# Optimization experiments

Measured on AMD Instinct MI355X. Metric: run time of the kernel, lower is better.

The kernel has to match this reference:

```python
import jax, jax.numpy as jnp
import numpy as np
import math

N, C, T, V = 8, 256, 128, 25
H, HC = 8, 32            # num_heads, head_channels
W, DIL = 3, 1            # window, dilation
O = 256                  # out_channels
PAD = (W + (W - 1) * (DIL - 1) - 1) // 2
B, L = N * T, W * V


def _ln(x, g, b):
    m = jnp.mean(x, -1, keepdims=True)
    v = jnp.var(x, -1, keepdims=True)
    return (x - m) * jax.lax.rsqrt(v + 1e-5) * g + b


def setup_inputs() -> dict:
    key = jax.random.key(0)
    ks = iter(jax.random.split(key, 40))
    def w(shape):
        return jax.random.normal(next(ks), shape, jnp.float32) * 0.02
    d = {"x": jax.random.normal(next(ks), (N, C, T, V), jnp.float32)}
    d.update(
        ln1_g=jnp.ones((C,)), ln1_b=jnp.zeros((C,)),
        Wq=w((C, C)), bq=jnp.zeros((C,)), Wqa=w((C, H)), bqa=jnp.zeros((H,)),
        Wk=w((C, C)), bk=jnp.zeros((C,)), Wka=w((C, H)), bka=jnp.zeros((H,)),
        Wv=w((C, C)), bv=jnp.zeros((C,)), Wt=w((C, C)), bt=jnp.zeros((C,)),
        Wp=w((C, C)), bp=jnp.zeros((C,)),
        ffn_g=jnp.ones((C,)), ffn_b=jnp.zeros((C,)),
        W1=w((C, C)), b1=jnp.zeros((C,)), W2=w((C, C)), b2=jnp.zeros((C,)),
        tn_g=jnp.ones((C,)), tn_b=jnp.zeros((C,)),
        c1_w=w((C, O)), c1_b=jnp.zeros((O,)),
        c2_w=w((W, O, O)), c2_b=jnp.zeros((O,)),
    )
    return d


def reference(x, ln1_g, ln1_b, Wq, bq, Wqa, bqa, Wk, bk, Wka, bka, Wv, bv,
              Wt, bt, Wp, bp, ffn_g, ffn_b, W1, b1, W2, b2, tn_g, tn_b,
              c1_w, c1_b, c2_w, c2_b):
    scale = 1.0 / math.sqrt(HC)
    # ---- Unfold over time: build window of frames around each t (nn.Unfold) ----
    xp = jnp.pad(x, ((0, 0), (0, 0), (PAD, PAD), (0, 0)))
    win = jnp.stack([jax.lax.dynamic_slice_in_dim(xp, k * DIL, T, 2) for k in range(W)], 2)  # (N,C,W,T,V)
    seq = win.transpose(0, 3, 2, 4, 1).reshape(B, L, C)  # (N*T, W*V, C)

    sep = lambda z: z.reshape(B, L, H, HC).transpose(0, 2, 1, 3)  # (B,H,L,HC)
    grp = lambda z: z.transpose(0, 2, 1, 3).reshape(B, -1, C)

    # ---- SpatioTemporalAttention (eval: dropouts off) ----
    nx = _ln(seq, ln1_g, ln1_b)
    q = nx @ Wq + bq                                            # (B,L,C)
    qw = jax.nn.softmax((q @ Wqa + bqa).transpose(0, 2, 1) * scale, axis=-1)  # (B,H,L)
    pq = jnp.einsum('bhl,bhlc->bhc', qw, sep(q)).reshape(B, 1, C)             # pooled query
    keys = nx @ Wk + bk
    kw = jax.nn.softmax(((keys * pq) @ Wka + bka).transpose(0, 2, 1) * scale, axis=-1)
    pk = jnp.einsum('bhl,bhlc->bhc', kw, sep(keys))             # pooled key (B,H,HC)
    vals = sep(nx @ Wv + bv)
    kv = grp(vals * pk[:, :, None, :]) @ Wt + bt                # (B,L,C)
    attn = (kv + q) @ Wp + bp                                   # residual-in-heads == plain add

    # ---- AttentionBranch residual + FFN ----
    att = attn + seq
    f = _ln(att, ffn_g, ffn_b)
    y = jax.nn.gelu(f @ W1 + b1, approximate=False) @ W2 + b2 + att  # (B,L,C)

    # ---- temporal branch: LN -> regroup frames -> 1x1 conv -> GELU -> (W,1) conv stride W ----
    t5 = _ln(y, tn_g, tn_b).reshape(N, T, W, V, C)
    h = jax.nn.gelu(t5 @ c1_w + c1_b, approximate=False)        # (N,T,W,V,O)
    out = jnp.einsum('ntwvi,wio->ntvo', h, c2_w) + c2_b         # stride==kernel conv == window contraction
    return out.transpose(0, 3, 1, 2)                            # (N,O,T,V)
```

## Files before the change

kernel.cpp:

```cpp
#include <hip/hip_runtime.h>


#define DI __device__ __forceinline__

constexpr int CC   = 256;
constexpr int CL   = 75;
constexpr int CV   = 25;
constexpr int CT   = 128;
constexpr int TP   = 130;
constexpr int MPAD = 8 * TP * CV;
constexpr int MBL  = 1024 * CL;
constexpr int MOUT = 8 * CT * CV;
constexpr float SM_SCALE = 0.17677669529663687f;

typedef __bf16 bf16x8 __attribute__((ext_vector_type(8)));
typedef float f32x4 __attribute__((ext_vector_type(4)));

DI float bf2f(unsigned short u) { return __uint_as_float(((unsigned)u) << 16); }
DI float bf2f_lo(unsigned u) { return __uint_as_float(u << 16); }
DI float bf2f_hi(unsigned u) { return __uint_as_float(u & 0xffff0000u); }
DI unsigned short f2bf(float f) {
  unsigned u = __float_as_uint(f);
  u += 0x7fffu + ((u >> 16) & 1u);
  return (unsigned short)(u >> 16);
}
DI unsigned packbf(float a, float b) {
  return (unsigned)f2bf(a) | ((unsigned)f2bf(b) << 16);
}
DI float geluf(float x) { return 0.5f * x * (1.f + erff(x * 0.70710678118654752440f)); }

DI void gll16(const unsigned short* g, unsigned short* l) {
  __builtin_amdgcn_global_load_lds(
      (const __attribute__((address_space(1))) unsigned int*)g,
      (__attribute__((address_space(3))) unsigned int*)l, 16, 0, 0);
}

DI int arow(int r) {
  int b = r / CL;
  int l = r - b * CL;
  int w = l / CV;
  int v = l - w * CV;
  int t = b & (CT - 1);
  int n = b >> 7;
  return (n * TP + t + w) * CV + v;
}

__global__ __launch_bounds__(256) void k_transpose(const float* __restrict__ x,
                                                   unsigned short* __restrict__ xtp) {
  __shared__ float tile[32][33];
  const int n = blockIdx.z;
  const int c0 = blockIdx.x * 32;
  const int tv0 = blockIdx.y * 32;
  const int tx = threadIdx.x & 31, ty = threadIdx.x >> 5;
#pragma unroll
  for (int j = 0; j < 32; j += 8) {
    tile[ty + j][tx] = x[((size_t)(n * CC + c0 + ty + j)) * 3200 + tv0 + tx];
  }
  __syncthreads();
#pragma unroll
  for (int j = 0; j < 32; j += 8) {
    int tv = tv0 + ty + j;
    int st = tv / CV, v = tv - st * CV;
    size_t row = ((size_t)n * TP + st + 1) * CV + v;
    xtp[row * CC + c0 + tx] = f2bf(tile[tx][ty + j]);
  }
}

__global__ __launch_bounds__(256) void k_zero_pad(unsigned short* __restrict__ xtp) {
  int i = blockIdx.x * 256 + threadIdx.x;
  int c = i & 255;
  int rid = i >> 8;
  int n = rid / 50;
  int rem = rid - n * 50;
  int side = rem / 25;
  int v = rem - side * 25;
  size_t row = ((size_t)n * TP + side * (TP - 1)) * CV + v;
  xtp[row * CC + c] = 0;
}

struct TJobs {
  const float* src[10];
  unsigned short* dst[10];
  int stride[10];
  int off[10];
};
__global__ __launch_bounds__(256) void k_wtrans(TJobs J) {
  __shared__ float tile[32][33];
  const int j = blockIdx.z;
  const float* src = J.src[j];
  unsigned short* dst = J.dst[j];
  const int stride = J.stride[j], off = J.off[j];
  const int k0 = blockIdx.x * 32, n0 = blockIdx.y * 32;
  const int tx = threadIdx.x & 31, ty = threadIdx.x >> 5;
#pragma unroll
  for (int jj = 0; jj < 32; jj += 8)
    tile[ty + jj][tx] = src[(size_t)(k0 + ty + jj) * 256 + n0 + tx];
  __syncthreads();
#pragma unroll
  for (int jj = 0; jj < 32; jj += 8)
    dst[(size_t)(n0 + ty + jj) * stride + off + k0 + tx] = f2bf(tile[tx][ty + jj]);
}

__global__ __launch_bounds__(256) void k_wtwp(const float* __restrict__ Wt,
                                              const float* __restrict__ Wp,
                                              unsigned short* __restrict__ fused) {
  __shared__ float wrow[256];
  const int k = blockIdx.x, n = threadIdx.x;
  wrow[n] = Wt[(size_t)k * 256 + n];
  __syncthreads();
  float acc = 0.f;
  for (int j = 0; j < 256; ++j) acc = fmaf(wrow[j], Wp[(size_t)j * 256 + n], acc);
  fused[(size_t)n * 512 + k] = f2bf(acc);
}

__global__ __launch_bounds__(256) void k_bias2(const float* __restrict__ bt,
                                               const float* __restrict__ Wp,
                                               const float* __restrict__ bp,
                                               const float* __restrict__ bq,
                                               const float* __restrict__ bk,
                                               const float* __restrict__ bv,
                                               float* __restrict__ bias2,
                                               float* __restrict__ bias3) {
  const int n = threadIdx.x;
  float acc = bp[n];
  for (int j = 0; j < 256; ++j) acc = fmaf(bt[j], Wp[(size_t)j * 256 + n], acc);
  bias2[n] = acc;
  bias3[n] = bq[n];
  bias3[256 + n] = bk[n];
  bias3[512 + n] = bv[n];
}

__global__ __launch_bounds__(256) void k_ln4(const unsigned short* __restrict__ X,
                                             const float* __restrict__ g,
                                             const float* __restrict__ b,
                                             unsigned short* __restrict__ Y) {
  const int row = blockIdx.x * 4 + (threadIdx.x >> 6);
  const int lane = threadIdx.x & 63;
  const uint2 u = *(const uint2*)(X + (size_t)row * CC + lane * 4);
  const float x0 = bf2f_lo(u.x), x1 = bf2f_hi(u.x), x2 = bf2f_lo(u.y), x3 = bf2f_hi(u.y);
  float s = x0 + x1 + x2 + x3;
  float q = x0 * x0 + x1 * x1 + x2 * x2 + x3 * x3;
#pragma unroll
  for (int o = 32; o; o >>= 1) { s += __shfl_xor(s, o); q += __shfl_xor(q, o); }
  const float mean = s * (1.f / CC);
  const float var = q * (1.f / CC) - mean * mean;
  const float rs = rsqrtf(var + 1e-5f);
  const float4 g4 = *(const float4*)(g + lane * 4);
  const float4 b4 = *(const float4*)(b + lane * 4);
  uint2 o2;
  o2.x = packbf((x0 - mean) * rs * g4.x + b4.x, (x1 - mean) * rs * g4.y + b4.y);
  o2.y = packbf((x2 - mean) * rs * g4.z + b4.z, (x3 - mean) * rs * g4.w + b4.w);
  *(uint2*)(Y + (size_t)row * CC + lane * 4) = o2;
}

template <int AMODE, int EPI, int KD, bool MULTI>
__global__ __launch_bounds__(512) void k_mgemm(const unsigned short* __restrict__ A,
                                               const unsigned short* __restrict__ BwT,
                                               const float* __restrict__ bias,
                                               unsigned short* __restrict__ Cout,
                                               float* __restrict__ FOut,
                                               int M) {
  if constexpr (MULTI) {
    const int z = blockIdx.y;
    BwT += (size_t)z * (256 * 256);
    bias += z * 256;
    Cout += (size_t)z * MPAD * CC;
  }
  __shared__ unsigned short SH[20480];
  const int tid = threadIdx.x;
  const int lane = tid & 63;
  const int wid = tid >> 6;
  const int wm = wid >> 2, wn = wid & 3;
  const int r0 = blockIdx.x * 64;
  f32x4 acc[2][4] = {};

  const bool sa = tid < 256;
  const int rA = r0 + (tid >> 2);
  const int rAc = (rA < M) ? rA : (M - 1);
  const int segs = ((tid & 3) ^ ((tid >> 3) & 3)) * 8;
  int hrb = 0;
  if (sa && AMODE == 4 && rA < M) {
    const int nb = rA / 3200, rr = rA - nb * 3200;
    const int tq = rr / 25, vq = rr - tq * 25;
    hrb = (nb * CT + tq) * CL + vq;
  }

  auto loadA4 = [&](int k0) -> uint4 {
    uint4 u = make_uint4(0, 0, 0, 0);
    if (!(sa && rA < M)) return u;
    const int w = k0 >> 8;
    u = *(const uint4*)(A + (size_t)(hrb + w * CV) * CC + (k0 & 255) + segs);
    return u;
  };
  auto stageB = [&](int buf, int k0) {
    unsigned short* bs = SH + 4096 + buf * 8192;
#pragma unroll
    for (int pp = 0; pp < 2; ++pp) {
      const int s = tid + pp * 512;
      const int cs = ((s & 3) ^ ((s >> 3) & 3)) * 8;
      gll16(BwT + (size_t)(s >> 2) * KD + k0 + cs, bs + s * 8);
    }
  };
  auto stageAg = [&](int buf, int k0) {
    if (sa) gll16(A + (size_t)rAc * CC + k0 + segs, SH + buf * 2048 + tid * 8);
  };
  const int swl = ((lane & 15) >> 1) & 3;
  auto mfmaStep = [&](int cur) {
    const unsigned short* as = SH + cur * 2048;
    const unsigned short* bs = SH + 4096 + cur * 8192;
    bf16x8 af[2], bfr[4];
#pragma unroll
    for (int mi = 0; mi < 2; ++mi)
      af[mi] = *(const bf16x8*)(as + (wm * 32 + mi * 16 + (lane & 15)) * 32 +
                                (((lane >> 4) ^ swl) * 8));
#pragma unroll
    for (int ni = 0; ni < 4; ++ni)
      bfr[ni] = *(const bf16x8*)(bs + (wn * 64 + ni * 16 + (lane & 15)) * 32 +
                                 (((lane >> 4) ^ swl) * 8));
#pragma unroll
    for (int mi = 0; mi < 2; ++mi)
#pragma unroll
      for (int ni = 0; ni < 4; ++ni)
        acc[mi][ni] = __builtin_amdgcn_mfma_f32_16x16x32_bf16(af[mi], bfr[ni], acc[mi][ni], 0, 0, 0);
  };

  constexpr int NT = KD / 32;
  if constexpr (AMODE == 0) {
    asm volatile("s_waitcnt vmcnt(0)" ::: "memory");
    stageB(0, 0);
    stageAg(0, 0);
    for (int t = 0; t < NT; ++t) {
      const int cur = t & 1;
      const bool more = (t + 1 < NT);
      if (more) { stageB(cur ^ 1, (t + 1) * 32); stageAg(cur ^ 1, (t + 1) * 32); }
      if (wid < 4) {
        if (more) asm volatile("s_waitcnt vmcnt(3)" ::: "memory");
        else      asm volatile("s_waitcnt vmcnt(0)" ::: "memory");
      } else {
        if (more) asm volatile("s_waitcnt vmcnt(2)" ::: "memory");
        else      asm volatile("s_waitcnt vmcnt(0)" ::: "memory");
      }
      __builtin_amdgcn_s_barrier();
      asm volatile("" ::: "memory");
      mfmaStep(cur);
      asm volatile("s_waitcnt lgkmcnt(0)" ::: "memory");
      __builtin_amdgcn_s_barrier();
      asm volatile("" ::: "memory");
    }
    __syncthreads();
  } else {
    {
      const uint4 a0 = loadA4(0);
      stageB(0, 0);
      if (sa) *(uint4*)(SH + tid * 8) = a0;
    }
    for (int t = 0; t < NT; ++t) {
      const int cur = t & 1;
      const bool more = (t + 1 < NT);
      if (more) {
        const uint4 an = loadA4((t + 1) * 32);
        stageB(cur ^ 1, (t + 1) * 32);
        if (sa) *(uint4*)(SH + (cur ^ 1) * 2048 + tid * 8) = an;
      }
      asm volatile("s_waitcnt lgkmcnt(0)" ::: "memory");
      if (more) asm volatile("s_waitcnt vmcnt(2)" ::: "memory");
      else      asm volatile("s_waitcnt vmcnt(0)" ::: "memory");
      __builtin_amdgcn_s_barrier();
      asm volatile("" ::: "memory");
      mfmaStep(cur);
      asm volatile("s_waitcnt lgkmcnt(0)" ::: "memory");
      __builtin_amdgcn_s_barrier();
      asm volatile("" ::: "memory");
    }
    if constexpr (EPI == 0) __syncthreads();
  }

  const int ln15 = lane & 15, lq = lane >> 4;
  if constexpr (EPI == 4) {
#pragma unroll
    for (int mi = 0; mi < 2; ++mi) {
#pragma unroll
      for (int ni = 0; ni < 4; ++ni) {
        const int col = wn * 64 + ni * 16 + ln15;
        const float bcol = bias[col];
        const int rbase = r0 + wm * 32 + mi * 16 + lq * 4;
        const int nb = rbase / 3200, rr = rbase - nb * 3200;
        float4 v;
        v.x = acc[mi][ni][0] + bcol;
        v.y = acc[mi][ni][1] + bcol;
        v.z = acc[mi][ni][2] + bcol;
        v.w = acc[mi][ni][3] + bcol;
        *(float4*)(FOut + (size_t)nb * 819200 + (size_t)col * 3200 + rr) = v;
      }
    }
  } else {
    constexpr int LDC = 260;
#pragma unroll
    for (int mi = 0; mi < 2; ++mi) {
#pragma unroll
      for (int ni = 0; ni < 4; ++ni) {
        const int col = wn * 64 + ni * 16 + ln15;
        const float bcol = bias[col];
#pragma unroll
        for (int rg = 0; rg < 4; ++rg) {
          const int lrow = wm * 32 + mi * 16 + lq * 4 + rg;
          SH[lrow * LDC + col] = f2bf(acc[mi][ni][rg] + bcol);
        }
      }
    }
    __syncthreads();
#pragma unroll
    for (int i = 0; i < 4; ++i) {
      const int idx = tid + i * 512;
      const int row = idx >> 5, ch = idx & 31;
      const int gr = r0 + row;
      if (gr < M)
        *(uint4*)(Cout + (size_t)gr * CC + ch * 8) = *(const uint4*)&SH[row * LDC + ch * 8];
    }
  }
}

__global__ __launch_bounds__(512, 4) void k_chain(
    const unsigned short* __restrict__ VP, const unsigned short* __restrict__ QP,
    const float* __restrict__ PK, const unsigned short* __restrict__ XTP,
    const unsigned short* __restrict__ fusedB, const float* __restrict__ bias2,
    const unsigned short* __restrict__ W1T, const float* __restrict__ b1,
    const unsigned short* __restrict__ W2T, const float* __restrict__ b2,
    const float* __restrict__ ffn_g, const float* __restrict__ ffn_b,
    const unsigned short* __restrict__ c1wT, const float* __restrict__ c1b,
    const float* __restrict__ tn_g, const float* __restrict__ tn_b,
    unsigned short* __restrict__ Hout) {
  constexpr int LDC = 264;
  __shared__ unsigned short SH[16896 + 4096 + 16384];
  unsigned short* ACT = SH;
  unsigned short* AS = SH + 16896;
  unsigned short* BS = SH + 16896 + 4096;
  const int tid = threadIdx.x;
  const int lane = tid & 63, wid = tid >> 6;
  const int wm = wid >> 2, wn = wid & 3;
  const int ln15 = lane & 15, lq = lane >> 4;
  const int swl = (ln15 >> 1) & 3;
  const int r0 = blockIdx.x * 64;

  const bool sa = tid < 256;
  const int rA = r0 + (tid >> 2);
  const int segs = ((tid & 3) ^ ((tid >> 3) & 3)) * 8;
  int ar = 0, bb = 0;
  if (sa) { ar = arow(rA); bb = rA / CL; }
  int xrow[8];
#pragma unroll
  for (int i = 0; i < 8; ++i)
    xrow[i] = arow(r0 + wm * 32 + (i >> 2) * 16 + lq * 4 + (i & 3));

  auto stageB = [&](const unsigned short* BwT, int KD, int buf, int k0) {
    unsigned short* bs = BS + buf * 8192;
#pragma unroll
    for (int pp = 0; pp < 2; ++pp) {
      const int s = tid + pp * 512;
      const int cs = ((s & 3) ^ ((s >> 3) & 3)) * 8;
      gll16(BwT + (size_t)(s >> 2) * KD + k0 + cs, bs + s * 8);
    }
  };
  auto loadA5 = [&](int k0) -> uint4 {
    uint4 u = make_uint4(0, 0, 0, 0);
    if (!sa) return u;
    if (k0 < 256) {
      const int kg = k0 + segs;
      const uint4 t4 = *(const uint4*)(VP + (size_t)ar * CC + kg);
      const float* sv = PK + bb * CC + kg;
      const float4 s0 = *(const float4*)sv;
      const float4 s1 = *(const float4*)(sv + 4);
      u.x = packbf(bf2f_lo(t4.x) * s0.x, bf2f_hi(t4.x) * s0.y);
      u.y = packbf(bf2f_lo(t4.y) * s0.z, bf2f_hi(t4.y) * s0.w);
      u.z = packbf(bf2f_lo(t4.z) * s1.x, bf2f_hi(t4.z) * s1.y);
      u.w = packbf(bf2f_lo(t4.w) * s1.z, bf2f_hi(t4.w) * s1.w);
    } else {
      u = *(const uint4*)(QP + (size_t)ar * CC + (k0 - 256) + segs);
    }
    return u;
  };
  auto ln_inplace = [&](const float* g, const float* b) {
    const float4 g4 = *(const float4*)(g + lane * 4);
    const float4 b4 = *(const float4*)(b + lane * 4);
#pragma unroll
    for (int rr = 0; rr < 8; ++rr) {
      const int row = wid * 8 + rr;
      const uint2 u = *(const uint2*)(ACT + row * LDC + lane * 4);
      const float x0 = bf2f_lo(u.x), x1 = bf2f_hi(u.x);
      const float x2 = bf2f_lo(u.y), x3 = bf2f_hi(u.y);
      float s = x0 + x1 + x2 + x3;
      float q = x0 * x0 + x1 * x1 + x2 * x2 + x3 * x3;
#pragma unroll
      for (int o = 32; o; o >>= 1) { s += __shfl_xor(s, o); q += __shfl_xor(q, o); }
      const float mean = s * (1.f / CC);
      const float var = q * (1.f / CC) - mean * mean;
      const float rs = rsqrtf(var + 1e-5f);
      uint2 o2;
      o2.x = packbf((x0 - mean) * rs * g4.x + b4.x, (x1 - mean) * rs * g4.y + b4.y);
      o2.y = packbf((x2 - mean) * rs * g4.z + b4.z, (x3 - mean) * rs * g4.w + b4.w);
      *(uint2*)(ACT + row * LDC + lane * 4) = o2;
    }
  };
  auto gemmACT = [&](const unsigned short* BwT, f32x4 (&a)[2][4], bool prestaged) {
    if (!prestaged) {
      asm volatile("s_waitcnt vmcnt(0)" ::: "memory");
      stageB(BwT, 256, 0, 0);
    }
    for (int t = 0; t < 8; ++t) {
      const int cur = t & 1;
      const bool more = (t + 1 < 8);
      if (more) stageB(BwT, 256, cur ^ 1, (t + 1) * 32);
      bf16x8 af[2];
#pragma unroll
      for (int mi = 0; mi < 2; ++mi)
        af[mi] = *(const bf16x8*)(ACT + (wm * 32 + mi * 16 + ln15) * LDC + t * 32 + lq * 8);
      if (more) asm volatile("s_waitcnt vmcnt(2)" ::: "memory");
      else      asm volatile("s_waitcnt vmcnt(0)" ::: "memory");
      __builtin_amdgcn_s_barrier();
      asm volatile("" ::: "memory");
      bf16x8 bfr[4];
#pragma unroll
      for (int ni = 0; ni < 4; ++ni)
        bfr[ni] = *(const bf16x8*)(BS + cur * 8192 + (wn * 64 + ni * 16 + ln15) * 32 +
                                   ((lq ^ swl) * 8));
#pragma unroll
      for (int mi = 0; mi < 2; ++mi)
#pragma unroll
        for (int ni = 0; ni < 4; ++ni)
          a[mi][ni] = __builtin_amdgcn_mfma_f32_16x16x32_bf16(af[mi], bfr[ni], a[mi][ni], 0, 0, 0);
      asm volatile("s_waitcnt lgkmcnt(0)" ::: "memory");
      __builtin_amdgcn_s_barrier();
      asm volatile("" ::: "memory");
    }
  };

  f32x4 acc[2][4] = {};
  {
    const uint4 a0 = loadA5(0);
    stageB(fusedB, 512, 0, 0);
    if (sa) *(uint4*)(AS + tid * 8) = a0;
  }
  for (int t = 0; t < 16; ++t) {
    const int cur = t & 1;
    const bool more = (t + 1 < 16);
    if (more) {
      const uint4 an = loadA5((t + 1) * 32);
      stageB(fusedB, 512, cur ^ 1, (t + 1) * 32);
      if (sa) *(uint4*)(AS + (cur ^ 1) * 2048 + tid * 8) = an;
    }
    asm volatile("s_waitcnt lgkmcnt(0)" ::: "memory");
    if (more) asm volatile("s_waitcnt vmcnt(2)" ::: "memory");
    else      asm volatile("s_waitcnt vmcnt(0)" ::: "memory");
    __builtin_amdgcn_s_barrier();
    asm volatile("" ::: "memory");
    {
      bf16x8 af[2], bfr[4];
#pragma unroll
      for (int mi = 0; mi < 2; ++mi)
        af[mi] = *(const bf16x8*)(AS + cur * 2048 + (wm * 32 + mi * 16 + ln15) * 32 +
                                  ((lq ^ swl) * 8));
#pragma unroll
      for (int ni = 0; ni < 4; ++ni)
        bfr[ni] = *(const bf16x8*)(BS + cur * 8192 + (wn * 64 + ni * 16 + ln15) * 32 +
                                   ((lq ^ swl) * 8));
#pragma unroll
      for (int mi = 0; mi < 2; ++mi)
#pragma unroll
        for (int ni = 0; ni < 4; ++ni)
          acc[mi][ni] = __builtin_amdgcn_mfma_f32_16x16x32_bf16(af[mi], bfr[ni], acc[mi][ni], 0, 0, 0);
    }
    asm volatile("s_waitcnt lgkmcnt(0)" ::: "memory");
    __builtin_amdgcn_s_barrier();
    asm volatile("" ::: "memory");
  }
  stageB(W1T, 256, 0, 0);
  f32x4 attres[2][4];
#pragma unroll
  for (int mi = 0; mi < 2; ++mi) {
#pragma unroll
    for (int ni = 0; ni < 4; ++ni) {
      const int col = wn * 64 + ni * 16 + ln15;
      const float bcol = bias2[col];
#pragma unroll
      for (int rg = 0; rg < 4; ++rg) {
        attres[mi][ni][rg] =
            acc[mi][ni][rg] + bcol + bf2f(XTP[(size_t)xrow[mi * 4 + rg] * CC + col]);
        ACT[(wm * 32 + mi * 16 + lq * 4 + rg) * LDC + col] = f2bf(attres[mi][ni][rg]);
      }
    }
  }
  __syncthreads();
  ln_inplace(ffn_g, ffn_b);
  __syncthreads();

  f32x4 acc2[2][4] = {};
  gemmACT(W1T, acc2, true);
  stageB(W2T, 256, 0, 0);
  __syncthreads();
#pragma unroll
  for (int mi = 0; mi < 2; ++mi)
#pragma unroll
    for (int ni = 0; ni < 4; ++ni) {
      const int col = wn * 64 + ni * 16 + ln15;
      const float bcol = b1[col];
#pragma unroll
      for (int rg = 0; rg < 4; ++rg)
        ACT[(wm * 32 + mi * 16 + lq * 4 + rg) * LDC + col] = f2bf(geluf(acc2[mi][ni][rg] + bcol));
    }
  __syncthreads();

  f32x4 acc3[2][4] = {};
  gemmACT(W2T, acc3, true);
  stageB(c1wT, 256, 0, 0);
  __syncthreads();
#pragma unroll
  for (int mi = 0; mi < 2; ++mi)
#pragma unroll
    for (int ni = 0; ni < 4; ++ni) {
      const int col = wn * 64 + ni * 16 + ln15;
      const float bcol = b2[col];
#pragma unroll
      for (int rg = 0; rg < 4; ++rg)
        ACT[(wm * 32 + mi * 16 + lq * 4 + rg) * LDC + col] =
            f2bf(acc3[mi][ni][rg] + bcol + attres[mi][ni][rg]);
    }
  __syncthreads();
  ln_inplace(tn_g, tn_b);
  __syncthreads();

  f32x4 acc4[2][4] = {};
  gemmACT(c1wT, acc4, true);
  __syncthreads();
#pragma unroll
  for (int mi = 0; mi < 2; ++mi)
#pragma unroll
    for (int ni = 0; ni < 4; ++ni) {
      const int col = wn * 64 + ni * 16 + ln15;
      const float bcol = c1b[col];
#pragma unroll
      for (int rg = 0; rg < 4; ++rg)
        ACT[(wm * 32 + mi * 16 + lq * 4 + rg) * LDC + col] = f2bf(geluf(acc4[mi][ni][rg] + bcol));
    }
  __syncthreads();
#pragma unroll
  for (int i = 0; i < 4; ++i) {
    const int idx = tid + i * 512;
    const int row = idx >> 5, ch = idx & 31;
    *(uint4*)(Hout + (size_t)(r0 + row) * CC + ch * 8) = *(const uint4*)&ACT[row * LDC + ch * 8];
  }
}

__global__ __launch_bounds__(256) void k_attpool2(
    const unsigned short* __restrict__ QPr, const unsigned short* __restrict__ KPr,
    const float* __restrict__ Wqa, const float* __restrict__ bqa,
    const float* __restrict__ Wka, const float* __restrict__ bka,
    float* __restrict__ PK) {
  __shared__ unsigned short rows[CL * CC];
  __shared__ float uu[8 * 258];
  __shared__ float lg[8 * 76];
  __shared__ float inv8[8];
  __shared__ float pq[256];
  __shared__ int arl[CL];
  const int b = blockIdx.x;
  const int t = threadIdx.x;

  if (t < CL) arl[t] = arow(b * CL + t);
  __syncthreads();

  auto dot_phase = [&](const float* b8) {
    const int c0 = (t & 63) * 4;
    for (int i = t; i < CL * 8; i += 256) {
      const int h = i / CL, l = i - h * CL;
      float acc = b8[h];
#pragma unroll 4
      for (int jj = 0; jj < CC; jj += 4) {
        const int c = (c0 + jj) & 255;
        const uint2 pr = *(const uint2*)&rows[l * CC + c];
        acc = fmaf(bf2f_lo(pr.x), uu[h * 258 + c], acc);
        acc = fmaf(bf2f_hi(pr.x), uu[h * 258 + c + 1], acc);
        acc = fmaf(bf2f_lo(pr.y), uu[h * 258 + c + 2], acc);
        acc = fmaf(bf2f_hi(pr.y), uu[h * 258 + c + 3], acc);
      }
      lg[h * 76 + l] = acc * SM_SCALE;
    }
  };
  auto softmax8 = [&]() {
    if (t < 8) {
      float m = -1e30f;
      for (int l = 0; l < CL; ++l) m = fmaxf(m, lg[t * 76 + l]);
      float s = 0.f;
      for (int l = 0; l < CL; ++l) {
        const float e = __expf(lg[t * 76 + l] - m);
        lg[t * 76 + l] = e;
        s += e;
      }
      inv8[t] = 1.f / s;
    }
  };

  for (int i = t; i < CL * 32; i += 256) {
    const int r = i >> 5, seg = i & 31;
    gll16(QPr + (size_t)arl[r] * CC + seg * 8, &rows[i * 8]);
  }
  for (int i = t; i < CC * 8; i += 256) {
    const int c = i >> 3, h = i & 7;
    uu[h * 258 + c] = Wqa[c * 8 + h];
  }
  __syncthreads();
  dot_phase(bqa);
  __syncthreads();
  softmax8();
  __syncthreads();
  {
    const int h = t >> 5;
    float acc = 0.f;
    for (int l = 0; l < CL; ++l) acc = fmaf(lg[h * 76 + l], bf2f(rows[l * CC + t]), acc);
    pq[t] = acc * inv8[h];
  }
  __syncthreads();

  for (int i = t; i < CL * 32; i += 256) {
    const int r = i >> 5, seg = i & 31;
    gll16(KPr + (size_t)arl[r] * CC + seg * 8, &rows[i * 8]);
  }
  for (int i = t; i < CC * 8; i += 256) {
    const int c = i >> 3, h = i & 7;
    uu[h * 258 + c] = pq[c] * Wka[c * 8 + h];
  }
  __syncthreads();
  dot_phase(bka);
  __syncthreads();
  softmax8();
  __syncthreads();
  {
    const int h = t >> 5;
    float acc = 0.f;
    for (int l = 0; l < CL; ++l) acc = fmaf(lg[h * 76 + l], bf2f(rows[l * CC + t]), acc);
    PK[(size_t)b * CC + t] = acc * inv8[h];
  }
}

extern "C" void kernel_launch(void* const* d_in, const int* in_sizes, int n_in,
                              void* d_out, int out_size, void* d_ws, size_t ws_size,
                              hipStream_t stream) {
  const float* x = (const float*)d_in[0];
  const float* ln1_g = (const float*)d_in[1];
  const float* ln1_b = (const float*)d_in[2];
  const float* Wq = (const float*)d_in[3];
  const float* bq = (const float*)d_in[4];
  const float* Wqa = (const float*)d_in[5];
  const float* bqa = (const float*)d_in[6];
  const float* Wk = (const float*)d_in[7];
  const float* bk = (const float*)d_in[8];
  const float* Wka = (const float*)d_in[9];
  const float* bka = (const float*)d_in[10];
  const float* Wv = (const float*)d_in[11];
  const float* bv = (const float*)d_in[12];
  const float* Wt = (const float*)d_in[13];
  const float* bt = (const float*)d_in[14];
  const float* Wp = (const float*)d_in[15];
  const float* bp = (const float*)d_in[16];
  const float* ffn_g = (const float*)d_in[17];
  const float* ffn_b = (const float*)d_in[18];
  const float* W1 = (const float*)d_in[19];
  const float* b1 = (const float*)d_in[20];
  const float* W2 = (const float*)d_in[21];
  const float* b2 = (const float*)d_in[22];
  const float* tn_g = (const float*)d_in[23];
  const float* tn_b = (const float*)d_in[24];
  const float* c1w = (const float*)d_in[25];
  const float* c1b = (const float*)d_in[26];
  const float* c2w = (const float*)d_in[27];
  const float* c2b = (const float*)d_in[28];
  float* out = (float*)d_out;

  char* wp = (char*)d_ws;
  auto alloc = [&](size_t bytes) -> char* {
    char* p = wp;
    wp += (bytes + 255) & ~(size_t)255;
    return p;
  };
  unsigned short* XTP = (unsigned short*)alloc((size_t)MPAD * CC * 2);
  unsigned short* LNXP = (unsigned short*)alloc((size_t)MPAD * CC * 2);
  unsigned short* QKVP = (unsigned short*)alloc((size_t)3 * MPAD * CC * 2);
  unsigned short* QP = QKVP;
  unsigned short* KP = QKVP + (size_t)MPAD * CC;
  unsigned short* VP = QKVP + (size_t)2 * MPAD * CC;
  unsigned short* Hb = (unsigned short*)alloc((size_t)MBL * CC * 2);
  float* PK = (float*)alloc((size_t)1024 * CC * 4);
  unsigned short* WqkvT = (unsigned short*)alloc((size_t)3 * 256 * 256 * 2);
  unsigned short* W1T = (unsigned short*)alloc(256 * 256 * 2);
  unsigned short* W2T = (unsigned short*)alloc(256 * 256 * 2);
  unsigned short* c1wT = (unsigned short*)alloc(256 * 256 * 2);
  unsigned short* c2wT = (unsigned short*)alloc(256 * 768 * 2);
  unsigned short* fusedB = (unsigned short*)alloc(256 * 512 * 2);
  float* bias2 = (float*)alloc(256 * 4);
  float* bias3 = (float*)alloc(768 * 4);

  TJobs J;
  const float* srcs[10] = {Wq, Wk, Wv, W1, W2, c1w, c2w, c2w + 65536, c2w + 131072, Wp};
  unsigned short* dsts[10] = {WqkvT, WqkvT + 65536, WqkvT + 131072, W1T, W2T, c1wT,
                              c2wT, c2wT, c2wT, fusedB};
  const int strides[10] = {256, 256, 256, 256, 256, 256, 768, 768, 768, 512};
  const int offs[10] = {0, 0, 0, 0, 0, 0, 0, 256, 512, 256};
  for (int i = 0; i < 10; ++i) {
    J.src[i] = srcs[i]; J.dst[i] = dsts[i]; J.stride[i] = strides[i]; J.off[i] = offs[i];
  }
  k_wtrans<<<dim3(8, 8, 10), 256, 0, stream>>>(J);
  k_wtwp<<<256, 256, 0, stream>>>(Wt, Wp, fusedB);
  k_bias2<<<1, 256, 0, stream>>>(bt, Wp, bp, bq, bk, bv, bias2, bias3);

  k_transpose<<<dim3(8, 100, 8), 256, 0, stream>>>(x, XTP);
  k_zero_pad<<<400, 256, 0, stream>>>(XTP);
  k_ln4<<<MPAD / 4, 256, 0, stream>>>(XTP, ln1_g, ln1_b, LNXP);

  const int gP = (MPAD + 63) / 64;
  const int gO = MOUT / 64;
  k_mgemm<0, 0, 256, true><<<dim3(gP, 3), 512, 0, stream>>>(
      LNXP, WqkvT, bias3, QKVP, nullptr, MPAD);

  k_attpool2<<<1024, 256, 0, stream>>>(QP, KP, Wqa, bqa, Wka, bka, PK);

  k_chain<<<MBL / 64, 512, 0, stream>>>(VP, QP, PK, XTP, fusedB, bias2,
                                        W1T, b1, W2T, b2, ffn_g, ffn_b,
                                        c1wT, c1b, tn_g, tn_b, Hb);

  k_mgemm<4, 4, 768, false><<<gO, 512, 0, stream>>>(Hb, c2wT, c2b, nullptr, out, MOUT);
}
```

Before: 265.7 us.

## Precompute q·Wp in the deduplicated QKV GEMM to halve the chain GEMM K

Folds Wq·Wp into a fourth output slice of the padded-frame QKV projection, with bias bq·Wp, so the q@Wp contribution is computed once per padded frame row rather than per windowed row. The attention chain GEMM's K dimension drops from 512 to 256, and the precomputed term is added from memory in the residual epilogue. This adds a larger QKV GEMM grid, an extra bf16 intermediate buffer and read, and a slight change in rounding.

```diff
diff --git a/kernel.cpp b/kernel.cpp
--- a/kernel.cpp
+++ b/kernel.cpp
@@ -79,10 +79,10 @@
 }
 
 struct TJobs {
-  const float* src[10];
-  unsigned short* dst[10];
-  int stride[10];
-  int off[10];
+  const float* src[9];
+  unsigned short* dst[9];
+  int stride[9];
+  int off[9];
 };
 __global__ __launch_bounds__(256) void k_wtrans(TJobs J) {
   __shared__ float tile[32][33];
@@ -102,15 +102,19 @@
 }
 
 __global__ __launch_bounds__(256) void k_wtwp(const float* __restrict__ Wt,
+                                              const float* __restrict__ Wq,
                                               const float* __restrict__ Wp,
-                                              unsigned short* __restrict__ fused) {
+                                              unsigned short* __restrict__ fusedB,
+                                              unsigned short* __restrict__ WqWpT) {
   __shared__ float wrow[256];
   const int k = blockIdx.x, n = threadIdx.x;
-  wrow[n] = Wt[(size_t)k * 256 + n];
+  const float* src = blockIdx.y ? Wq : Wt;
+  unsigned short* dst = blockIdx.y ? WqWpT : fusedB;
+  wrow[n] = src[(size_t)k * 256 + n];
   __syncthreads();
   float acc = 0.f;
   for (int j = 0; j < 256; ++j) acc = fmaf(wrow[j], Wp[(size_t)j * 256 + n], acc);
-  fused[(size_t)n * 512 + k] = f2bf(acc);
+  dst[(size_t)n * 256 + k] = f2bf(acc);
 }
 
 __global__ __launch_bounds__(256) void k_bias2(const float* __restrict__ bt,
@@ -123,11 +127,17 @@
                                                float* __restrict__ bias3) {
   const int n = threadIdx.x;
   float acc = bp[n];
-  for (int j = 0; j < 256; ++j) acc = fmaf(bt[j], Wp[(size_t)j * 256 + n], acc);
+  float accq = 0.f;
+  for (int j = 0; j < 256; ++j) {
+    const float w = Wp[(size_t)j * 256 + n];
+    acc = fmaf(bt[j], w, acc);
+    accq = fmaf(bq[j], w, accq);
+  }
   bias2[n] = acc;
   bias3[n] = bq[n];
   bias3[256 + n] = bk[n];
   bias3[512 + n] = bv[n];
+  bias3[768 + n] = accq;
 }
 
 __global__ __launch_bounds__(256) void k_ln4(const unsigned short* __restrict__ X,
@@ -321,8 +331,8 @@
 }
 
 __global__ __launch_bounds__(512, 4) void k_chain(
-    const unsigned short* __restrict__ VP, const unsigned short* __restrict__ QP,
-    const float* __restrict__ PK, const unsigned short* __restrict__ XTP,
+    const unsigned short* __restrict__ VP, const float* __restrict__ PK,
+    const unsigned short* __restrict__ XTP, const unsigned short* __restrict__ QWPP,
     const unsigned short* __restrict__ fusedB, const float* __restrict__ bias2,
     const unsigned short* __restrict__ W1T, const float* __restrict__ b1,
     const unsigned short* __restrict__ W2T, const float* __restrict__ b2,
@@ -364,19 +374,15 @@
   auto loadA5 = [&](int k0) -> uint4 {
     uint4 u = make_uint4(0, 0, 0, 0);
     if (!sa) return u;
-    if (k0 < 256) {
-      const int kg = k0 + segs;
-      const uint4 t4 = *(const uint4*)(VP + (size_t)ar * CC + kg);
-      const float* sv = PK + bb * CC + kg;
-      const float4 s0 = *(const float4*)sv;
-      const float4 s1 = *(const float4*)(sv + 4);
-      u.x = packbf(bf2f_lo(t4.x) * s0.x, bf2f_hi(t4.x) * s0.y);
-      u.y = packbf(bf2f_lo(t4.y) * s0.z, bf2f_hi(t4.y) * s0.w);
-      u.z = packbf(bf2f_lo(t4.z) * s1.x, bf2f_hi(t4.z) * s1.y);
-      u.w = packbf(bf2f_lo(t4.w) * s1.z, bf2f_hi(t4.w) * s1.w);
-    } else {
-      u = *(const uint4*)(QP + (size_t)ar * CC + (k0 - 256) + segs);
-    }
+    const int kg = k0 + segs;
+    const uint4 t4 = *(const uint4*)(VP + (size_t)ar * CC + kg);
+    const float* sv = PK + bb * CC + kg;
+    const float4 s0 = *(const float4*)sv;
+    const float4 s1 = *(const float4*)(sv + 4);
+    u.x = packbf(bf2f_lo(t4.x) * s0.x, bf2f_hi(t4.x) * s0.y);
+    u.y = packbf(bf2f_lo(t4.y) * s0.z, bf2f_hi(t4.y) * s0.w);
+    u.z = packbf(bf2f_lo(t4.z) * s1.x, bf2f_hi(t4.z) * s1.y);
+    u.w = packbf(bf2f_lo(t4.w) * s1.z, bf2f_hi(t4.w) * s1.w);
     return u;
   };
   auto ln_inplace = [&](const float* g, const float* b) {
@@ -437,15 +443,15 @@
   f32x4 acc[2][4] = {};
   {
     const uint4 a0 = loadA5(0);
-    stageB(fusedB, 512, 0, 0);
+    stageB(fusedB, 256, 0, 0);
     if (sa) *(uint4*)(AS + tid * 8) = a0;
   }
-  for (int t = 0; t < 16; ++t) {
+  for (int t = 0; t < 8; ++t) {
     const int cur = t & 1;
-    const bool more = (t + 1 < 16);
+    const bool more = (t + 1 < 8);
     if (more) {
       const uint4 an = loadA5((t + 1) * 32);
-      stageB(fusedB, 512, cur ^ 1, (t + 1) * 32);
+      stageB(fusedB, 256, cur ^ 1, (t + 1) * 32);
       if (sa) *(uint4*)(AS + (cur ^ 1) * 2048 + tid * 8) = an;
     }
     asm volatile("s_waitcnt lgkmcnt(0)" ::: "memory");
@@ -483,8 +489,8 @@
       const float bcol = bias2[col];
 #pragma unroll
       for (int rg = 0; rg < 4; ++rg) {
-        attres[mi][ni][rg] =
-            acc[mi][ni][rg] + bcol + bf2f(XTP[(size_t)xrow[mi * 4 + rg] * CC + col]);
+        const size_t ro = (size_t)xrow[mi * 4 + rg] * CC + col;
+        attres[mi][ni][rg] = acc[mi][ni][rg] + bcol + bf2f(QWPP[ro]) + bf2f(XTP[ro]);
         ACT[(wm * 32 + mi * 16 + lq * 4 + rg) * LDC + col] = f2bf(attres[mi][ni][rg]);
       }
     }
@@ -682,32 +688,33 @@
   };
   unsigned short* XTP = (unsigned short*)alloc((size_t)MPAD * CC * 2);
   unsigned short* LNXP = (unsigned short*)alloc((size_t)MPAD * CC * 2);
-  unsigned short* QKVP = (unsigned short*)alloc((size_t)3 * MPAD * CC * 2);
+  unsigned short* QKVP = (unsigned short*)alloc((size_t)4 * MPAD * CC * 2);
   unsigned short* QP = QKVP;
   unsigned short* KP = QKVP + (size_t)MPAD * CC;
   unsigned short* VP = QKVP + (size_t)2 * MPAD * CC;
+  unsigned short* QWPP = QKVP + (size_t)3 * MPAD * CC;
   unsigned short* Hb = (unsigned short*)alloc((size_t)MBL * CC * 2);
   float* PK = (float*)alloc((size_t)1024 * CC * 4);
-  unsigned short* WqkvT = (unsigned short*)alloc((size_t)3 * 256 * 256 * 2);
+  unsigned short* WqkvT = (unsigned short*)alloc((size_t)4 * 256 * 256 * 2);
   unsigned short* W1T = (unsigned short*)alloc(256 * 256 * 2);
   unsigned short* W2T = (unsigned short*)alloc(256 * 256 * 2);
   unsigned short* c1wT = (unsigned short*)alloc(256 * 256 * 2);
   unsigned short* c2wT = (unsigned short*)alloc(256 * 768 * 2);
-  unsigned short* fusedB = (unsigned short*)alloc(256 * 512 * 2);
+  unsigned short* fusedB = (unsigned short*)alloc(256 * 256 * 2);
   float* bias2 = (float*)alloc(256 * 4);
-  float* bias3 = (float*)alloc(768 * 4);
+  float* bias3 = (float*)alloc(1024 * 4);
 
   TJobs J;
-  const float* srcs[10] = {Wq, Wk, Wv, W1, W2, c1w, c2w, c2w + 65536, c2w + 131072, Wp};
-  unsigned short* dsts[10] = {WqkvT, WqkvT + 65536, WqkvT + 131072, W1T, W2T, c1wT,
-                              c2wT, c2wT, c2wT, fusedB};
-  const int strides[10] = {256, 256, 256, 256, 256, 256, 768, 768, 768, 512};
-  const int offs[10] = {0, 0, 0, 0, 0, 0, 0, 256, 512, 256};
-  for (int i = 0; i < 10; ++i) {
+  const float* srcs[9] = {Wq, Wk, Wv, W1, W2, c1w, c2w, c2w + 65536, c2w + 131072};
+  unsigned short* dsts[9] = {WqkvT, WqkvT + 65536, WqkvT + 131072, W1T, W2T, c1wT,
+                             c2wT, c2wT, c2wT};
+  const int strides[9] = {256, 256, 256, 256, 256, 256, 768, 768, 768};
+  const int offs[9] = {0, 0, 0, 0, 0, 0, 0, 256, 512};
+  for (int i = 0; i < 9; ++i) {
     J.src[i] = srcs[i]; J.dst[i] = dsts[i]; J.stride[i] = strides[i]; J.off[i] = offs[i];
   }
-  k_wtrans<<<dim3(8, 8, 10), 256, 0, stream>>>(J);
-  k_wtwp<<<256, 256, 0, stream>>>(Wt, Wp, fusedB);
+  k_wtrans<<<dim3(8, 8, 9), 256, 0, stream>>>(J);
+  k_wtwp<<<dim3(256, 2), 256, 0, stream>>>(Wt, Wq, Wp, fusedB, WqkvT + 3 * 65536);
   k_bias2<<<1, 256, 0, stream>>>(bt, Wp, bp, bq, bk, bv, bias2, bias3);
 
   k_transpose<<<dim3(8, 100, 8), 256, 0, stream>>>(x, XTP);
@@ -716,12 +723,12 @@
 
   const int gP = (MPAD + 63) / 64;
   const int gO = MOUT / 64;
-  k_mgemm<0, 0, 256, true><<<dim3(gP, 3), 512, 0, stream>>>(
+  k_mgemm<0, 0, 256, true><<<dim3(gP, 4), 512, 0, stream>>>(
       LNXP, WqkvT, bias3, QKVP, nullptr, MPAD);
 
   k_attpool2<<<1024, 256, 0, stream>>>(QP, KP, Wqa, bqa, Wka, bka, PK);
 
-  k_chain<<<MBL / 64, 512, 0, stream>>>(VP, QP, PK, XTP, fusedB, bias2,
+  k_chain<<<MBL / 64, 512, 0, stream>>>(VP, PK, XTP, QWPP, fusedB, bias2,
                                         W1T, b1, W2T, b2, ffn_g, ffn_b,
                                         c1wT, c1b, tn_g, tn_b, Hb);
 
```

Result: faster. 260.2 us (-2.1%).
